# Optimization experiments

Hardware: AMD Instinct MI355X
Metric: run time of the kernel (lower is better)

The kernel has to match this reference:

```python
import jax, jax.numpy as jnp
import numpy as np

# Module constants from init_kwargs
N_X_AXIS = 128
N_Y_AXIS = 128
X_RANGE = (-10.0, 10.0)
Y_RANGE = (-10.0, 10.0)
LOG_L_SCALE = 0.0  # log(1.0), requires_grad=False
N_CTX = 20000


def make_grid():
    # Give_2d_Grid(min_x=x_range[0], max_x=x_range[1], min_y=y_range[1], max_y=y_range[0], flatten=True)
    # -> flattened (G,2) grid; row index i*N_Y_AXIS + j holds [x_i, y_j],
    # with y running from y_range[1] down to y_range[0] (note the swapped args in the source).
    xs = jnp.linspace(X_RANGE[0], X_RANGE[1], N_X_AXIS)
    ys = jnp.linspace(Y_RANGE[1], Y_RANGE[0], N_Y_AXIS)
    gx, gy = jnp.meshgrid(xs, ys, indexing='ij')  # (N_X, N_Y)
    return jnp.stack([gx, gy], axis=-1).reshape(-1, 2)  # (G, 2)


def setup_inputs() -> dict:
    key = jax.random.key(0)
    k1, k2 = jax.random.split(key)
    X = jax.random.normal(k1, (N_CTX, 2), dtype=jnp.float32) * 3.0  # context locations
    Y = jax.random.normal(k2, (N_CTX, 2), dtype=jnp.float32)        # context vectors
    return {"X": X, "Y": Y}


def reference(X, Y):
    # l_scale = exp(clamp(log_l_scale, -5, 5))
    l_scale = jnp.exp(jnp.clip(jnp.asarray(LOG_L_SCALE, X.dtype), -5.0, 5.0))
    grid = make_grid().astype(X.dtype)  # (G, 2)

    # RBF Gram matrix between grid and context points: exp(-||g - x||^2 / (2 l^2))
    # computed via the expanded-square trick to keep it a GEMM + elementwise.
    g2 = jnp.sum(grid * grid, axis=1, keepdims=True)        # (G, 1)
    x2 = jnp.sum(X * X, axis=1, keepdims=True).T            # (1, n)
    d2 = g2 + x2 - 2.0 * (grid @ X.T)                        # (G, n)
    Gram = jnp.exp(-d2 / (2.0 * l_scale * l_scale))          # (G, n)

    # Psi(Y): prepend a ones column -> (n, 3)
    Expand_Y = jnp.concatenate([jnp.ones((Y.shape[0], 1), Y.dtype), Y], axis=1)

    Feature_Map = Gram @ Expand_Y                            # (G, 3)

    # normalize smoothing channels by density channel
    density = Feature_Map[:, :1]
    Norm = jnp.concatenate([density, Feature_Map[:, 1:] / density], axis=1)

    # (G,3) -> (N_X, N_Y, 3) -> permute(2,1,0) -> (3, N_Y, N_X) -> (1, 3, N_Y, N_X)
    out = Norm.reshape(N_X_AXIS, N_Y_AXIS, 3).transpose(2, 1, 0)[None]
    return out
```

## Files before the change

kernel.cpp:

```cpp
#include <hip/hip_runtime.h>


#define NXA 128
#define NG  16384
#define NC  20000
#define KC  32
#define LDA 34
#define NSL 128
#define SLEN 157

#define STEP (20.0f / 127.0f)
#define KNEG (-0.72134752044448170368f)

typedef _Float16 v8h  __attribute__((ext_vector_type(8)));
typedef float    v16f __attribute__((ext_vector_type(16)));
typedef float    v4f  __attribute__((ext_vector_type(4)));

__device__ __forceinline__ float fast_exp2(float x) {
    return __builtin_amdgcn_exp2f(x);
}

__global__ __launch_bounds__(256) void k_mfma(const float* __restrict__ X,
                                              const float* __restrict__ Y,
                                              float* __restrict__ fm) {
    __shared__ _Float16 Ag[32 * LDA];
    __shared__ _Float16 Bm[384 * LDA];
    __shared__ float    Xs[KC * 2];
    __shared__ float    Ys[KC * 2];

    const int t     = threadIdx.x;
    const int p     = blockIdx.x;
    const int slice = blockIdx.y;
    const int n0    = slice * SLEN;
    int nEnd = n0 + SLEN; if (nEnd > NC) nEnd = NC;

    const int lane = t & 63, wave = t >> 6;
    const int l31 = lane & 31, lh = lane >> 5;

    v16f acc[3];
#pragma unroll
    for (int m = 0; m < 3; ++m) acc[m] = (v16f)(0.f);

    for (int c0 = n0; c0 < nEnd; c0 += KC) {
        __syncthreads();
        if (t < KC) {
            int n = c0 + t;
            float2 xv = (n < NC) ? *(const float2*)(X + 2 * n)
                                 : make_float2(1e19f, 1e19f);
            float2 yv = (n < NC) ? *(const float2*)(Y + 2 * n)
                                 : make_float2(0.f, 0.f);
            if (n >= nEnd) { xv = make_float2(1e19f, 1e19f); yv = make_float2(0.f, 0.f); }
            Xs[2 * t] = xv.x; Xs[2 * t + 1] = xv.y;
            Ys[2 * t] = yv.x; Ys[2 * t + 1] = yv.y;
        }
        __syncthreads();

        {
            const int kg = t & 3;
            const int i0 = t >> 2;
            const float* xp = Xs + kg * 16;
            const float* yp = Ys + kg * 16;
#pragma unroll
            for (int pass = 0; pass < 2; ++pass) {
                int i = i0 + 64 * pass;
                float gx = -10.f + (float)i * STEP;
                v8h e, e1, e2;
#pragma unroll
                for (int u = 0; u < 8; ++u) {
                    float dx = gx - xp[2 * u];
                    float w  = fast_exp2(dx * dx * KNEG);
                    e[u]  = (_Float16)w;
                    e1[u] = (_Float16)(w * yp[2 * u]);
                    e2[u] = (_Float16)(w * yp[2 * u + 1]);
                }
                *(v8h*)(Bm + i * LDA + kg * 8)         = e;
                *(v8h*)(Bm + (128 + i) * LDA + kg * 8) = e1;
                *(v8h*)(Bm + (256 + i) * LDA + kg * 8) = e2;
            }
        }
        if (t < 128) {
            const int kg = t & 3;
            const int j  = t >> 2;
            float gy = 10.f - (float)(32 * p + j) * STEP;
            const float* xp = Xs + kg * 16;
            v8h e;
#pragma unroll
            for (int u = 0; u < 8; ++u) {
                float dy = gy - xp[2 * u + 1];
                e[u] = (_Float16)fast_exp2(dy * dy * KNEG);
            }
            *(v8h*)(Ag + j * LDA + kg * 8) = e;
        }
        __syncthreads();

#pragma unroll
        for (int s = 0; s < 2; ++s) {
            int k = s * 16 + lh * 8;
            v8h af = *(const v8h*)(Ag + l31 * LDA + k);
#pragma unroll
            for (int tn = 0; tn < 3; ++tn) {
                int n = wave * 96 + tn * 32 + l31;
                v8h bf = *(const v8h*)(Bm + n * LDA + k);
                acc[tn] = __builtin_amdgcn_mfma_f32_32x32x16_f16(af, bf, acc[tn], 0, 0, 0);
            }
        }
    }

    const size_t cstride = (size_t)NSL * NG;
#pragma unroll
    for (int tn = 0; tn < 3; ++tn) {
        int n = wave * 96 + tn * 32 + l31;
        int c = n >> 7, i = n & 127;
        float* base = fm + (size_t)c * cstride + (size_t)slice * NG + i;
#pragma unroll
        for (int r = 0; r < 16; ++r) {
            int j  = (r & 3) + 8 * (r >> 2) + 4 * lh;
            int gj = 32 * p + j;
            base[gj * NXA] = acc[tn][r];
        }
    }
}

__global__ __launch_bounds__(256) void k_reduce_norm(const float* __restrict__ fm,
                                                     float* __restrict__ out,
                                                     int nslice) {
    __shared__ v4f sAcc[3][16][16];
    const int q  = threadIdx.x & 15;
    const int sg = threadIdx.x >> 4;
    const int gp = blockIdx.x * 64 + q * 4;
    const size_t cstride = (size_t)nslice * NG;
    const int per = nslice >> 4;
    v4f w = (v4f)(0.f), pp = (v4f)(0.f), qq = (v4f)(0.f);
    int s0 = sg * per, s1 = s0 + per;
    for (int s = s0; s < s1; ++s) {
        const float* base = fm + (size_t)s * NG + gp;
        w  += *(const v4f*)(base);
        pp += *(const v4f*)(base + cstride);
        qq += *(const v4f*)(base + 2 * cstride);
    }
    sAcc[0][sg][q] = w; sAcc[1][sg][q] = pp; sAcc[2][sg][q] = qq;
    __syncthreads();
    if (threadIdx.x < 16) {
        const int c = threadIdx.x;
        v4f W = (v4f)(0.f), P = (v4f)(0.f), Q = (v4f)(0.f);
#pragma unroll
        for (int s = 0; s < 16; ++s) {
            W += sAcc[0][s][c]; P += sAcc[1][s][c]; Q += sAcc[2][s][c];
        }
        v4f inv; inv.x = 1.f / W.x; inv.y = 1.f / W.y;
        inv.z = 1.f / W.z; inv.w = 1.f / W.w;
        const int o = blockIdx.x * 64 + c * 4;
        *(v4f*)(out + o)          = W;
        *(v4f*)(out + NG + o)     = P * inv;
        *(v4f*)(out + 2 * NG + o) = Q * inv;
    }
}

__global__ __launch_bounds__(256) void k_accum_atomic(const float* __restrict__ X,
                                                      const float* __restrict__ Y,
                                                      float* __restrict__ dst,
                                                      int slice_len) {
    __shared__ float As[64 * 64], Bs[64 * 64], Yl[64 * 2];
    const int t = threadIdx.x, tx = t & 15, ty = t >> 4;
    const int pos = blockIdx.x;
    const int tI = (pos >> 1) * 64, tJ = (pos & 1) * 64;
    const int n0 = blockIdx.y * slice_len;
    int nEnd = n0 + slice_len; if (nEnd > NC) nEnd = NC;
    float aw[16], ap[16], aq[16];
#pragma unroll
    for (int k = 0; k < 16; ++k) { aw[k] = ap[k] = aq[k] = 0.f; }
    for (int c0 = n0; c0 < nEnd; c0 += 64) {
        __syncthreads();
#pragma unroll
        for (int k = 0; k < 16; ++k) {
            int l = k * 256 + t, nl = l >> 6, ii = l & 63, n = c0 + nl;
            float a = 0.f, b = 0.f;
            if (n < nEnd) {
                float dx = (-10.f + (float)(tI + ii) * STEP) - X[2 * n];
                float dy = (10.f - (float)(tJ + ii) * STEP) - X[2 * n + 1];
                a = fast_exp2(dx * dx * KNEG);
                b = fast_exp2(dy * dy * KNEG);
            }
            As[nl * 64 + ii] = a; Bs[nl * 64 + ii] = b;
        }
        if (t < 128) { int n = c0 + (t >> 1); Yl[t] = (n < nEnd) ? Y[2 * n + (t & 1)] : 0.f; }
        __syncthreads();
        int cnt = nEnd - c0; if (cnt > 64) cnt = 64;
        for (int n = 0; n < cnt; ++n) {
            const float4 a4 = *(const float4*)(As + n * 64 + tx * 4);
            const float4 b4 = *(const float4*)(Bs + n * 64 + ty * 4);
            float y0 = Yl[2 * n], y1 = Yl[2 * n + 1];
            float av[4] = {a4.x, a4.y, a4.z, a4.w};
            float bv[4] = {b4.x, b4.y, b4.z, b4.w};
#pragma unroll
            for (int di = 0; di < 4; ++di)
#pragma unroll
                for (int dj = 0; dj < 4; ++dj) {
                    int k = di * 4 + dj;
                    float w = av[di] * bv[dj];
                    aw[k] += w; ap[k] = fmaf(w, y0, ap[k]); aq[k] = fmaf(w, y1, aq[k]);
                }
        }
    }
#pragma unroll
    for (int di = 0; di < 4; ++di)
#pragma unroll
        for (int dj = 0; dj < 4; ++dj) {
            int gi = tI + tx * 4 + di, gj = tJ + ty * 4 + dj;
            int o = gj * NXA + gi, k = di * 4 + dj;
            atomicAdd(dst + o, aw[k]);
            atomicAdd(dst + NG + o, ap[k]);
            atomicAdd(dst + 2 * NG + o, aq[k]);
        }
}

__global__ __launch_bounds__(256) void k_norm_inplace(float* __restrict__ out) {
    int t = blockIdx.x * 256 + threadIdx.x;
    if (t >= NG) return;
    float inv = 1.f / out[t];
    out[NG + t] *= inv; out[2 * NG + t] *= inv;
}

extern "C" void kernel_launch(void* const* d_in, const int* in_sizes, int n_in,
                              void* d_out, int out_size, void* d_ws, size_t ws_size,
                              hipStream_t stream) {
    const float* X = (const float*)d_in[0];
    const float* Y = (const float*)d_in[1];
    float* out = (float*)d_out;
    const size_t need = (size_t)NSL * NG * 3 * sizeof(float);
    if (ws_size >= need) {
        float* fm = (float*)d_ws;
        k_mfma<<<dim3(4, NSL), 256, 0, stream>>>(X, Y, fm);
        k_reduce_norm<<<NG / 64, 256, 0, stream>>>(fm, out, NSL);
    } else {
        hipMemsetAsync(d_out, 0, (size_t)out_size * sizeof(float), stream);
        k_accum_atomic<<<dim3(4, 64), 256, 0, stream>>>(X, Y, out, (NC + 63) / 64);
        k_norm_inplace<<<(NG + 255) / 256, 256, 0, stream>>>(out);
    }
}
```

Measured before the change: 78.93 us.

## Register-prefetch context points, remove LDS staging, resize slices and reduce grid

Context slices now split evenly as 125 slices of 160 points in five exact 32-point chunks, so the boundary and padding checks go away. Each thread loads its X/Y values straight from global memory into registers, and the next chunk is prefetched while the current one is turned into exponentials. This drops the Xs/Ys shared staging and one barrier per chunk. The reduce kernel now uses twice as many blocks of 32 grid points each, with 32 slice groups, to raise parallelism. The cost is more registers per thread and redundant global loads across threads.

Measured after the change: 76.45 us. -3.1%, faster.

```diff
diff --git a/kernel.cpp b/kernel.cpp
--- a/kernel.cpp
+++ b/kernel.cpp
@@ -6,8 +6,9 @@
 #define NC  20000
 #define KC  32
 #define LDA 34
-#define NSL 128
-#define SLEN 157
+#define NSL 125
+#define SLEN 160
+#define NCHUNK 5
 
 #define STEP (20.0f / 127.0f)
 #define KNEG (-0.72134752044448170368f)
@@ -25,71 +26,88 @@
                                               float* __restrict__ fm) {
     __shared__ _Float16 Ag[32 * LDA];
     __shared__ _Float16 Bm[384 * LDA];
-    __shared__ float    Xs[KC * 2];
-    __shared__ float    Ys[KC * 2];
 
     const int t     = threadIdx.x;
     const int p     = blockIdx.x;
     const int slice = blockIdx.y;
     const int n0    = slice * SLEN;
-    int nEnd = n0 + SLEN; if (nEnd > NC) nEnd = NC;
 
     const int lane = t & 63, wave = t >> 6;
     const int l31 = lane & 31, lh = lane >> 5;
+    const int kg = t & 3;
+    const int i0 = t >> 2;
+    const float gx0 = -10.f + (float)i0 * STEP;
+    const float gx1 = -10.f + (float)(i0 + 64) * STEP;
+    const float gyj = 10.f - (float)(32 * p + (t >> 2)) * STEP;
+
+    const float4* Xp = (const float4*)X;
+    const float4* Yp = (const float4*)Y;
+    const int fb0 = (n0 >> 1) + kg * 4;
 
     v16f acc[3];
 #pragma unroll
     for (int m = 0; m < 3; ++m) acc[m] = (v16f)(0.f);
 
-    for (int c0 = n0; c0 < nEnd; c0 += KC) {
-        __syncthreads();
-        if (t < KC) {
-            int n = c0 + t;
-            float2 xv = (n < NC) ? *(const float2*)(X + 2 * n)
-                                 : make_float2(1e19f, 1e19f);
-            float2 yv = (n < NC) ? *(const float2*)(Y + 2 * n)
-                                 : make_float2(0.f, 0.f);
-            if (n >= nEnd) { xv = make_float2(1e19f, 1e19f); yv = make_float2(0.f, 0.f); }
-            Xs[2 * t] = xv.x; Xs[2 * t + 1] = xv.y;
-            Ys[2 * t] = yv.x; Ys[2 * t + 1] = yv.y;
-        }
-        __syncthreads();
+    float4 xf[4], yf[4];
+#pragma unroll
+    for (int q = 0; q < 4; ++q) { xf[q] = Xp[fb0 + q]; yf[q] = Yp[fb0 + q]; }
+
+#pragma unroll
+    for (int m = 0; m < NCHUNK; ++m) {
+        float4 xc[4], yc[4];
+#pragma unroll
+        for (int q = 0; q < 4; ++q) { xc[q] = xf[q]; yc[q] = yf[q]; }
+
+        __syncthreads();
+
+        if (m < NCHUNK - 1) {
+            int fb = fb0 + 16 * (m + 1);
+#pragma unroll
+            for (int q = 0; q < 4; ++q) { xf[q] = Xp[fb + q]; yf[q] = Yp[fb + q]; }
+        }
 
         {
-            const int kg = t & 3;
-            const int i0 = t >> 2;
-            const float* xp = Xs + kg * 16;
-            const float* yp = Ys + kg * 16;
-#pragma unroll
-            for (int pass = 0; pass < 2; ++pass) {
-                int i = i0 + 64 * pass;
-                float gx = -10.f + (float)i * STEP;
-                v8h e, e1, e2;
-#pragma unroll
-                for (int u = 0; u < 8; ++u) {
-                    float dx = gx - xp[2 * u];
-                    float w  = fast_exp2(dx * dx * KNEG);
-                    e[u]  = (_Float16)w;
-                    e1[u] = (_Float16)(w * yp[2 * u]);
-                    e2[u] = (_Float16)(w * yp[2 * u + 1]);
-                }
-                *(v8h*)(Bm + i * LDA + kg * 8)         = e;
-                *(v8h*)(Bm + (128 + i) * LDA + kg * 8) = e1;
-                *(v8h*)(Bm + (256 + i) * LDA + kg * 8) = e2;
-            }
+            float xu[8], y0u[8], y1u[8];
+#pragma unroll
+            for (int q = 0; q < 4; ++q) {
+                xu[2 * q]      = xc[q].x;  xu[2 * q + 1]  = xc[q].z;
+                y0u[2 * q]     = yc[q].x;  y0u[2 * q + 1] = yc[q].z;
+                y1u[2 * q]     = yc[q].y;  y1u[2 * q + 1] = yc[q].w;
+            }
+            v8h e, e1, e2;
+#pragma unroll
+            for (int u = 0; u < 8; ++u) {
+                float dx = gx0 - xu[u];
+                float w  = fast_exp2(dx * dx * KNEG);
+                e[u]  = (_Float16)w;
+                e1[u] = (_Float16)(w * y0u[u]);
+                e2[u] = (_Float16)(w * y1u[u]);
+            }
+            *(v8h*)(Bm + i0 * LDA + kg * 8)         = e;
+            *(v8h*)(Bm + (128 + i0) * LDA + kg * 8) = e1;
+            *(v8h*)(Bm + (256 + i0) * LDA + kg * 8) = e2;
+#pragma unroll
+            for (int u = 0; u < 8; ++u) {
+                float dx = gx1 - xu[u];
+                float w  = fast_exp2(dx * dx * KNEG);
+                e[u]  = (_Float16)w;
+                e1[u] = (_Float16)(w * y0u[u]);
+                e2[u] = (_Float16)(w * y1u[u]);
+            }
+            *(v8h*)(Bm + (64 + i0) * LDA + kg * 8)  = e;
+            *(v8h*)(Bm + (192 + i0) * LDA + kg * 8) = e1;
+            *(v8h*)(Bm + (320 + i0) * LDA + kg * 8) = e2;
         }
         if (t < 128) {
-            const int kg = t & 3;
-            const int j  = t >> 2;
-            float gy = 10.f - (float)(32 * p + j) * STEP;
-            const float* xp = Xs + kg * 16;
-            v8h e;
+            v8h a;
 #pragma unroll
             for (int u = 0; u < 8; ++u) {
-                float dy = gy - xp[2 * u + 1];
-                e[u] = (_Float16)fast_exp2(dy * dy * KNEG);
-            }
-            *(v8h*)(Ag + j * LDA + kg * 8) = e;
+                float x1u = (u & 1) ? ((u >> 1) == 0 ? xc[0].w : (u >> 1) == 1 ? xc[1].w : (u >> 1) == 2 ? xc[2].w : xc[3].w)
+                                    : ((u >> 1) == 0 ? xc[0].y : (u >> 1) == 1 ? xc[1].y : (u >> 1) == 2 ? xc[2].y : xc[3].y);
+                float dy = gyj - x1u;
+                a[u] = (_Float16)fast_exp2(dy * dy * KNEG);
+            }
+            *(v8h*)(Ag + (t >> 2) * LDA + kg * 8) = a;
         }
         __syncthreads();
 
@@ -122,16 +140,16 @@
 }
 
 __global__ __launch_bounds__(256) void k_reduce_norm(const float* __restrict__ fm,
-                                                     float* __restrict__ out,
-                                                     int nslice) {
-    __shared__ v4f sAcc[3][16][16];
-    const int q  = threadIdx.x & 15;
-    const int sg = threadIdx.x >> 4;
-    const int gp = blockIdx.x * 64 + q * 4;
-    const size_t cstride = (size_t)nslice * NG;
-    const int per = nslice >> 4;
+                                                     float* __restrict__ out) {
+    __shared__ v4f sAcc[3][32][8];
+    const int q  = threadIdx.x & 7;
+    const int sg = threadIdx.x >> 3;
+    const int gp = blockIdx.x * 32 + q * 4;
+    const size_t cstride = (size_t)NSL * NG;
+    const int per = (NSL + 31) >> 5;
+    int s0 = sg * per;
+    int s1 = s0 + per; if (s1 > NSL) s1 = NSL;
     v4f w = (v4f)(0.f), pp = (v4f)(0.f), qq = (v4f)(0.f);
-    int s0 = sg * per, s1 = s0 + per;
     for (int s = s0; s < s1; ++s) {
         const float* base = fm + (size_t)s * NG + gp;
         w  += *(const v4f*)(base);
@@ -140,16 +158,16 @@
     }
     sAcc[0][sg][q] = w; sAcc[1][sg][q] = pp; sAcc[2][sg][q] = qq;
     __syncthreads();
-    if (threadIdx.x < 16) {
+    if (threadIdx.x < 8) {
         const int c = threadIdx.x;
         v4f W = (v4f)(0.f), P = (v4f)(0.f), Q = (v4f)(0.f);
 #pragma unroll
-        for (int s = 0; s < 16; ++s) {
+        for (int s = 0; s < 32; ++s) {
             W += sAcc[0][s][c]; P += sAcc[1][s][c]; Q += sAcc[2][s][c];
         }
         v4f inv; inv.x = 1.f / W.x; inv.y = 1.f / W.y;
         inv.z = 1.f / W.z; inv.w = 1.f / W.w;
-        const int o = blockIdx.x * 64 + c * 4;
+        const int o = blockIdx.x * 32 + c * 4;
         *(v4f*)(out + o)          = W;
         *(v4f*)(out + NG + o)     = P * inv;
         *(v4f*)(out + 2 * NG + o) = Q * inv;
@@ -231,7 +249,7 @@
     if (ws_size >= need) {
         float* fm = (float*)d_ws;
         k_mfma<<<dim3(4, NSL), 256, 0, stream>>>(X, Y, fm);
-        k_reduce_norm<<<NG / 64, 256, 0, stream>>>(fm, out, NSL);
+        k_reduce_norm<<<NG / 32, 256, 0, stream>>>(fm, out);
     } else {
         hipMemsetAsync(d_out, 0, (size_t)out_size * sizeof(float), stream);
         k_accum_atomic<<<dim3(4, 64), 256, 0, stream>>>(X, Y, out, (NC + 63) / 64);
```
